# Kernel tuning notes

Measured on AMD Instinct MI355X. Metric: run time of the kernel, lower is better.

The kernel has to match this reference:

```python
import jax
import jax.numpy as jnp
from jax import lax
import numpy as np

# ---- static RPN config (mirrors init_kwargs) ----
STRIDES = (8, 16)
SIZES = ((32, 32), (16, 16))
SCALES = ((64.0 ** 2,), (128.0 ** 2,))
RATIOS = ((0.5, 1.0, 2.0), (0.5, 1.0, 2.0))
IMAGE_SIZE = (256, 256)
NMS_THRESH = 0.7
POST_NMS_TOP_N = 2000
NUM_LEVELS = 2
TOP_K_PER_LEVEL = POST_NMS_TOP_N // NUM_LEVELS  # padded NMS output slots per level


def _generate_anchors(stride, scales, ratios, size, image_size):
    """Anchors of shape (H*W*A, 4) in (x1,y1,x2,y2), clamped to image."""
    H, W = size
    cy = (np.arange(H, dtype=np.float32) + 0.5) * stride
    cx = (np.arange(W, dtype=np.float32) + 0.5) * stride
    ws, hs = [], []
    for s in scales:
        for r in ratios:
            ws.append(np.sqrt(s / r))
            hs.append(np.sqrt(s * r))
    ws = np.asarray(ws, np.float32)  # [A]
    hs = np.asarray(hs, np.float32)
    cxg, cyg = np.meshgrid(cx, cy)  # [H, W]
    x1 = cxg[..., None] - 0.5 * ws
    y1 = cyg[..., None] - 0.5 * hs
    x2 = cxg[..., None] + 0.5 * ws
    y2 = cyg[..., None] + 0.5 * hs
    a = np.stack([x1, y1, x2, y2], axis=-1)  # [H, W, A, 4]
    a[..., 0] = np.clip(a[..., 0], 0, image_size[0])
    a[..., 1] = np.clip(a[..., 1], 0, image_size[1])
    a[..., 2] = np.clip(a[..., 2], 0, image_size[0])
    a[..., 3] = np.clip(a[..., 3], 0, image_size[1])
    return a.reshape(-1, 4).astype(np.float32)


ANCHORS = [
    _generate_anchors(STRIDES[i], SCALES[i], RATIOS[i], SIZES[i], IMAGE_SIZE)
    for i in range(NUM_LEVELS)
]


def conv2d(x, w, b, padding):
    y = lax.conv_general_dilated(
        x, w, window_strides=(1, 1), padding=padding,
        dimension_numbers=("NCHW", "OIHW", "NCHW"))
    return y + b[None, :, None, None]


def decode_boxes(anchors, deltas):
    """Standard R-CNN box decode. anchors [N,4], deltas [..., N, 4]."""
    wa = anchors[:, 2] - anchors[:, 0]
    ha = anchors[:, 3] - anchors[:, 1]
    cxa = anchors[:, 0] + 0.5 * wa
    cya = anchors[:, 1] + 0.5 * ha
    dx, dy, dw, dh = deltas[..., 0], deltas[..., 1], deltas[..., 2], deltas[..., 3]
    cx = dx * wa + cxa
    cy = dy * ha + cya
    w = jnp.exp(dw) * wa
    h = jnp.exp(dh) * ha
    return jnp.stack([cx - 0.5 * w, cy - 0.5 * h, cx + 0.5 * w, cy + 0.5 * h], axis=-1)


def clamp_boxes(b):
    return jnp.stack([
        jnp.clip(b[..., 0], 0.0, IMAGE_SIZE[0]),
        jnp.clip(b[..., 1], 0.0, IMAGE_SIZE[1]),
        jnp.clip(b[..., 2], 0.0, IMAGE_SIZE[0]),
        jnp.clip(b[..., 3], 0.0, IMAGE_SIZE[1]),
    ], axis=-1)


def _pairwise_iou(b):
    # b: [N, 4] -> [N, N] IoU (torchvision convention, no +1)
    area = (b[:, 2] - b[:, 0]) * (b[:, 3] - b[:, 1])
    lt = jnp.maximum(b[:, None, :2], b[None, :, :2])
    rb = jnp.minimum(b[:, None, 2:], b[None, :, 2:])
    wh = jnp.clip(rb - lt, 0.0)
    inter = wh[..., 0] * wh[..., 1]
    return inter / (area[:, None] + area[None, :] - inter)


def nms_padded(boxes, scores, thresh, top_k):
    """Exact greedy NMS; returns (top_k,4) boxes and (top_k,) scores padded with -1."""
    N = boxes.shape[0]
    order = jnp.argsort(-scores)
    b = boxes[order]
    s = scores[order]
    iou = _pairwise_iou(b)  # [N, N]

    def body(supp, xs):
        row, i = xs
        keep_i = jnp.logical_not(supp[i])
        supp = supp | (keep_i & (row > thresh) & (jnp.arange(N) > i))
        return supp, keep_i

    _, keep = lax.scan(body, jnp.zeros((N,), bool), (iou, jnp.arange(N)))
    rank = jnp.cumsum(keep) - 1  # position among kept, in score order
    slot = jnp.where(keep & (rank < top_k), rank, top_k)  # overflow -> dump row
    out_b = jnp.full((top_k + 1, 4), -1.0, boxes.dtype).at[slot].set(b)
    out_s = jnp.full((top_k + 1,), -1.0, scores.dtype).at[slot].set(s)
    return out_b[:top_k], out_s[:top_k]


def _rpn_level(feat, anchors, conv_w, conv_b, cls_w, cls_b, reg_w, reg_b):
    x = jax.nn.relu(conv2d(feat, conv_w, conv_b, "SAME"))
    cls = conv2d(x, cls_w, cls_b, "VALID")              # [BS, A, H, W]
    reg = conv2d(x, reg_w, reg_b, "VALID")              # [BS, 4A, H, W]
    BS, A, H, W = cls.shape
    cls = cls.transpose(0, 2, 3, 1).reshape(BS, -1)                      # [BS, HWA]
    reg = reg.transpose(0, 2, 3, 1).reshape(BS, H, W, A, 4).reshape(BS, -1, 4)
    boxes = clamp_boxes(decode_boxes(anchors, lax.stop_gradient(reg)))   # [BS, HWA, 4]
    scores = jax.nn.sigmoid(lax.stop_gradient(cls))                      # [BS, HWA]
    kb, ks = jax.vmap(lambda bb, ss: nms_padded(bb, ss, NMS_THRESH, TOP_K_PER_LEVEL))(boxes, scores)
    return kb, ks


def setup_inputs() -> dict:
    key = jax.random.key(0)
    ks = jax.random.split(key, 5)
    C = 256
    A = 3
    return {
        "feat0": jax.random.normal(ks[0], (4, C, 32, 32), jnp.float32),
        "feat1": jax.random.normal(ks[1], (4, C, 16, 16), jnp.float32),
        "conv_w": 0.01 * jax.random.normal(ks[2], (C, C, 3, 3), jnp.float32),
        "conv_b": jnp.zeros((C,), jnp.float32),
        "cls_w": 0.01 * jax.random.normal(ks[3], (A, C, 1, 1), jnp.float32),
        "cls_b": jnp.zeros((A,), jnp.float32),
        "reg_w": 0.01 * jax.random.normal(ks[4], (4 * A, C, 1, 1), jnp.float32),
        "reg_b": jnp.zeros((4 * A,), jnp.float32),
    }


def reference(feat0, feat1, conv_w, conv_b, cls_w, cls_b, reg_w, reg_b):
    feats = [feat0, feat1]
    kb_all, ks_all = [], []
    for i in range(NUM_LEVELS):
        kb, ks = _rpn_level(feats[i], jnp.asarray(ANCHORS[i]),
                            conv_w, conv_b, cls_w, cls_b, reg_w, reg_b)
        kb_all.append(kb)
        ks_all.append(ks)
    bboxes = jnp.concatenate(kb_all, axis=1)   # [BS, POST_NMS_TOP_N, 4]
    scores = jnp.concatenate(ks_all, axis=1)   # [BS, POST_NMS_TOP_N]
    idx = jnp.argsort(-scores, axis=1)         # descending; -1 pads go last
    bboxes = jnp.take_along_axis(bboxes, idx[..., None], axis=1)
    return bboxes
```

## Files before the change

kernel.cpp:

```cpp
#include <hip/hip_runtime.h>
#include <math.h>


__global__ __launch_bounds__(256, 4) void conv3_sk_u(
    const float* __restrict__ feat0, const float* __restrict__ feat1,
    const float* __restrict__ conv_w,
    double* __restrict__ part0, double* __restrict__ part1)
{
  __shared__ float Ald[2][16][64];
  __shared__ float Bld[2][16][64];
  const int t = threadIdx.x;
  const int bid = blockIdx.x;
  const float* feat;
  double* part;
  int oc_t, p_t, k_base, hw_sh, w_sh, H;
  if (bid < 1024) {
    int kc = bid >> 8;
    feat = feat0; part = part0 + (size_t)kc * 4096 * 256;
    oc_t = bid & 3; p_t = (bid >> 2) & 63;
    k_base = kc * 576; hw_sh = 10; w_sh = 5; H = 32;
  } else {
    int b2 = bid - 1024;
    int kc = b2 >> 6;
    feat = feat1; part = part1 + (size_t)kc * 1024 * 256;
    oc_t = b2 & 3; p_t = (b2 >> 2) & 15;
    k_base = kc * 576; hw_sh = 8; w_sh = 4; H = 16;
  }
  const int oc_base = oc_t * 64;
  const int p_base  = p_t * 64;
  const int wmask = H - 1, hwmask = (1 << hw_sh) - 1;
  const int skk = t >> 4;
  const int q4  = (t & 15) * 4;

  float a_r[4], b_r[4];
  auto load_tile = [&](int kt) {
    const int k0 = k_base + kt * 16;
    const float* wrow = conv_w + (size_t)(oc_base + q4) * 2304 + (k0 + skk);
#pragma unroll
    for (int u = 0; u < 4; ++u) a_r[u] = wrow[(size_t)u * 2304];
    int p = p_base + q4;
    int b = p >> hw_sh, pin = p & hwmask;
    int y = pin >> w_sh, x0 = pin & wmask;
    int k = k0 + skk;
    int ic = k / 9, rr = k - ic * 9;
    int ky = rr / 3, kx = rr - ky * 3;
    int iy = y + ky - 1;
    const float* frow = feat + (((b << 8) + ic) << hw_sh) + (iy << w_sh);
    bool yok = (unsigned)iy < (unsigned)H;
#pragma unroll
    for (int u = 0; u < 4; ++u) {
      int ix = x0 + u + kx - 1;
      b_r[u] = (yok && (unsigned)ix < (unsigned)H) ? frow[ix] : 0.f;
    }
  };

  const int ty4 = (t >> 4) * 4;
  const int tx4 = (t & 15) * 4;
  double acc[4][4] = {};

  load_tile(0);
  for (int kt = 0; kt < 36; ++kt) {
    const int buf = kt & 1;
    *(float4*)&Ald[buf][skk][q4] = make_float4(a_r[0], a_r[1], a_r[2], a_r[3]);
    *(float4*)&Bld[buf][skk][q4] = make_float4(b_r[0], b_r[1], b_r[2], b_r[3]);
    __syncthreads();
    if (kt + 1 < 36) load_tile(kt + 1);
#pragma unroll
    for (int kk = 0; kk < 16; ++kk) {
      float4 av = *(const float4*)&Ald[buf][kk][ty4];
      float4 bv = *(const float4*)&Bld[buf][kk][tx4];
      double ad[4] = {(double)av.x, (double)av.y, (double)av.z, (double)av.w};
      double bd[4] = {(double)bv.x, (double)bv.y, (double)bv.z, (double)bv.w};
#pragma unroll
      for (int i = 0; i < 4; ++i)
#pragma unroll
        for (int j = 0; j < 4; ++j) acc[i][j] += ad[i] * bd[j];
    }
  }
#pragma unroll
  for (int j = 0; j < 4; ++j) {
    int p = p_base + tx4 + j;
    double* row = part + (size_t)p * 256 + oc_base + ty4;
    *(double2*)&row[0] = make_double2(acc[0][j], acc[1][j]);
    *(double2*)&row[2] = make_double2(acc[2][j], acc[3][j]);
  }
}

__global__ __launch_bounds__(256) void rhd_k(
    const double* __restrict__ part0, const double* __restrict__ part1,
    const float* __restrict__ conv_b,
    const float* __restrict__ cls_w, const float* __restrict__ cls_b,
    const float* __restrict__ reg_w, const float* __restrict__ reg_b,
    float* __restrict__ box0, float* __restrict__ sc0,
    float* __restrict__ box1, float* __restrict__ sc1)
{
  int wid = (blockIdx.x * 256 + threadIdx.x) >> 6;
  int lane = threadIdx.x & 63;
  int lvl = wid >= 4096;
  const double* part = lvl ? part1 : part0;
  int p = lvl ? wid - 4096 : wid;
  int M = lvl ? 1024 : 4096;
  double s4[4];
  {
    float4 bv = ((const float4*)conv_b)[lane];
    s4[0] = (double)bv.x; s4[1] = (double)bv.y;
    s4[2] = (double)bv.z; s4[3] = (double)bv.w;
  }
#pragma unroll
  for (int ks = 0; ks < 4; ++ks) {
    const double2* pr = (const double2*)(part + (size_t)ks * M * 256 + (size_t)p * 256);
    double2 a = pr[2 * lane], b = pr[2 * lane + 1];
    s4[0] += a.x; s4[1] += a.y; s4[2] += b.x; s4[3] += b.y;
  }
  float xv[4];
#pragma unroll
  for (int q = 0; q < 4; ++q) {
    float f = (float)s4[q];
    xv[q] = f > 0.f ? f : 0.f;
  }
  double acc[15];
#pragma unroll
  for (int o = 0; o < 15; ++o) {
    const float* wr = (o < 3) ? (cls_w + o * 256) : (reg_w + (o - 3) * 256);
    float4 wv = ((const float4*)wr)[lane];
    acc[o] = (double)wv.x * (double)xv[0] + (double)wv.y * (double)xv[1] +
             (double)wv.z * (double)xv[2] + (double)wv.w * (double)xv[3];
  }
#pragma unroll
  for (int d = 1; d < 64; d <<= 1)
#pragma unroll
    for (int o = 0; o < 15; ++o)
      acc[o] += __shfl_xor(acc[o], d, 64);
  if (lane < 3) {
    int a = lane;
    float cls = (float)(acc[a] + (double)cls_b[a]);
    float score = 1.f / (1.f + expf(-cls));
    float dx = (float)(acc[3 + a * 4 + 0] + (double)reg_b[a * 4 + 0]);
    float dy = (float)(acc[3 + a * 4 + 1] + (double)reg_b[a * 4 + 1]);
    float dw = (float)(acc[3 + a * 4 + 2] + (double)reg_b[a * 4 + 2]);
    float dh = (float)(acc[3 + a * 4 + 3] + (double)reg_b[a * 4 + 3]);
    int hw_sh = lvl ? 8 : 10, w_sh = lvl ? 4 : 5, Wd = lvl ? 16 : 32;
    float S = lvl ? 16.f : 8.f;
    double scale = lvl ? 16384.0 : 4096.0;
    int b = p >> hw_sh, pin = p & ((1 << hw_sh) - 1);
    int y = pin >> w_sh, x = pin & (Wd - 1);
    double ratio = (a == 0) ? 0.5 : (a == 1 ? 1.0 : 2.0);
    float w_a = (float)sqrt(scale / ratio);
    float h_a = (float)sqrt(scale * ratio);
    float cx = ((float)x + 0.5f) * S;
    float cy = ((float)y + 0.5f) * S;
    float x1 = cx - 0.5f * w_a, y1 = cy - 0.5f * h_a;
    float x2 = cx + 0.5f * w_a, y2 = cy + 0.5f * h_a;
    x1 = fminf(fmaxf(x1, 0.f), 256.f); y1 = fminf(fmaxf(y1, 0.f), 256.f);
    x2 = fminf(fmaxf(x2, 0.f), 256.f); y2 = fminf(fmaxf(y2, 0.f), 256.f);
    float wa = x2 - x1, ha = y2 - y1;
    float cxa = x1 + 0.5f * wa, cya = y1 + 0.5f * ha;
    float ncx = dx * wa + cxa;
    float ncy = dy * ha + cya;
    float nw = expf(dw) * wa;
    float nh = expf(dh) * ha;
    float bx1 = ncx - 0.5f * nw, by1 = ncy - 0.5f * nh;
    float bx2 = ncx + 0.5f * nw, by2 = ncy + 0.5f * nh;
    bx1 = fminf(fmaxf(bx1, 0.f), 256.f); by1 = fminf(fmaxf(by1, 0.f), 256.f);
    bx2 = fminf(fmaxf(bx2, 0.f), 256.f); by2 = fminf(fmaxf(by2, 0.f), 256.f);
    int n = pin * 3 + a;
    if (lvl) {
      ((float4*)box1)[(size_t)b * 768 + n] = make_float4(bx1, by1, bx2, by2);
      sc1[b * 768 + n] = score;
    } else {
      ((float4*)box0)[(size_t)b * 3072 + n] = make_float4(bx1, by1, bx2, by2);
      sc0[b * 3072 + n] = score;
    }
  }
}

__global__ __launch_bounds__(256) void sort_level_k(
    const float* __restrict__ sc0, const float* __restrict__ box0,
    float* __restrict__ ssc0, float* __restrict__ sbox0,
    const float* __restrict__ sc1, const float* __restrict__ box1,
    float* __restrict__ ssc1, float* __restrict__ sbox1)
{
  __shared__ __align__(16) float s[3072];
  int z = blockIdx.x;
  const float *sc, *box; float *ssc, *sbox; int N, b, c;
  if (z < 48) { sc = sc0; box = box0; ssc = ssc0; sbox = sbox0; N = 3072; b = z / 12; c = z % 12; }
  else { int z2 = z - 48; sc = sc1; box = box1; ssc = ssc1; sbox = sbox1; N = 768; b = z2 / 3; c = z2 % 3; }
  const float* scb = sc + (size_t)b * N;
  for (int j = threadIdx.x; j < N; j += 256) s[j] = scb[j];
  __syncthreads();
  int i = c * 256 + threadIdx.x;
  float si = s[i];
  int rank = 0;
  const float4* sv = (const float4*)s;
  for (int j4 = 0; j4 < (N >> 2); ++j4) {
    float4 v = sv[j4];
    int j = j4 * 4;
    rank += (v.x > si) || (v.x == si && (j + 0) < i);
    rank += (v.y > si) || (v.y == si && (j + 1) < i);
    rank += (v.z > si) || (v.z == si && (j + 2) < i);
    rank += (v.w > si) || (v.w == si && (j + 3) < i);
  }
  ssc[(size_t)b * N + rank] = si;
  float4 bi = ((const float4*)box)[(size_t)b * N + i];
  ((float4*)sbox)[(size_t)b * N + rank] = bi;
}

__global__ __launch_bounds__(256) void mask_col_k(
    const float* __restrict__ sbox0, const float* __restrict__ sbox1,
    unsigned long long* __restrict__ mask0, unsigned long long* __restrict__ mask1,
    unsigned long long* __restrict__ colD0, unsigned long long* __restrict__ colD1)
{
  int bid = blockIdx.x;
  if (bid < 2448) {
    __shared__ float4 bj[64];
    const float* sbox; unsigned long long* mask; int N, words, w, i_ch, b;
    if (bid < 2304) {
      sbox = sbox0; mask = mask0; N = 3072; words = 48;
      w = bid % 48; int r = bid / 48; i_ch = r % 12; b = r / 12;
    } else {
      int z = bid - 2304;
      sbox = sbox1; mask = mask1; N = 768; words = 12;
      w = z % 12; int r = z / 12; i_ch = r % 3; b = r / 3;
    }
    int i = i_ch * 256 + threadIdx.x;
    if (threadIdx.x < 64)
      bj[threadIdx.x] = ((const float4*)sbox)[(size_t)b * N + w * 64 + threadIdx.x];
    __syncthreads();
    float4 bi = ((const float4*)sbox)[(size_t)b * N + i];
    float ai = (bi.z - bi.x) * (bi.w - bi.y);
    unsigned long long m = 0ull;
#pragma unroll 16
    for (int jj = 0; jj < 64; ++jj) {
      int j = w * 64 + jj;
      float4 bv = bj[jj];
      float lx = fmaxf(bi.x, bv.x), ly = fmaxf(bi.y, bv.y);
      float rx = fminf(bi.z, bv.z), ry = fminf(bi.w, bv.w);
      float iw = fmaxf(rx - lx, 0.f), ih = fmaxf(ry - ly, 0.f);
      float inter = iw * ih;
      float aj = (bv.z - bv.x) * (bv.w - bv.y);
      float iou = inter / (ai + aj - inter);
      if ((iou > 0.7f) & (j > i)) m |= (1ull << jj);
    }
    mask[((size_t)b * N + i) * words + w] = m;
  } else {
    __shared__ float4 tb[4][64];
    int sub = threadIdx.x >> 6, lane = threadIdx.x & 63;
    const float* sbox; unsigned long long* colD; int N, tile, b;
    if (bid < 2496) {
      int unit = (bid - 2448) * 4 + sub;
      sbox = sbox0; colD = colD0; N = 3072;
      tile = unit % 48; b = unit / 48;
    } else {
      int unit = (bid - 2496) * 4 + sub;
      sbox = sbox1; colD = colD1; N = 768;
      tile = unit % 12; b = unit / 12;
    }
    tb[sub][lane] = ((const float4*)sbox)[(size_t)b * N + tile * 64 + lane];
    __syncthreads();
    float4 bq = tb[sub][lane];
    float aq = (bq.z - bq.x) * (bq.w - bq.y);
    unsigned long long col = 0ull;
#pragma unroll 16
    for (int ii = 0; ii < 64; ++ii) {
      float4 bi = tb[sub][ii];
      float lx = fmaxf(bq.x, bi.x), ly = fmaxf(bq.y, bi.y);
      float rx = fminf(bq.z, bi.z), ry = fminf(bq.w, bi.w);
      float iw = fmaxf(rx - lx, 0.f), ih = fmaxf(ry - ly, 0.f);
      float inter = iw * ih;
      float ai = (bi.z - bi.x) * (bi.w - bi.y);
      float iou = inter / (aq + ai - inter);
      if ((iou > 0.7f) & (lane > ii)) col |= (1ull << ii);
    }
    colD[(size_t)b * N + tile * 64 + lane] = col;
  }
}

__global__ __launch_bounds__(64) void nms_scan_k(
    const float* __restrict__ ssc0, const float* __restrict__ sbox0,
    const unsigned long long* __restrict__ mask0,
    const unsigned long long* __restrict__ colD0,
    const float* __restrict__ ssc1, const float* __restrict__ sbox1,
    const unsigned long long* __restrict__ mask1,
    const unsigned long long* __restrict__ colD1,
    float* __restrict__ cb, float* __restrict__ cs)
{
  int z = blockIdx.x;
  int lvl = z >> 2, b = z & 3;
  int N = lvl ? 768 : 3072;
  int words = lvl ? 12 : 48;
  const float* ssc = (lvl ? ssc1 : ssc0) + (size_t)b * N;
  const float4* sbox = ((const float4*)(lvl ? sbox1 : sbox0)) + (size_t)b * N;
  const unsigned long long* mask = (lvl ? mask1 : mask0) + (size_t)b * N * words;
  const unsigned long long* colD = (lvl ? colD1 : colD0) + (size_t)b * N;
  const int lane = threadIdx.x;
  float* csb = cs + (size_t)b * 2000 + lvl * 1000;
  float4* cbb = (float4*)(cb + ((size_t)b * 2000 + lvl * 1000) * 4);
  for (int q = lane; q < 1000; q += 64) {
    csb[q] = -1.f;
    cbb[q] = make_float4(-1.f, -1.f, -1.f, -1.f);
  }
  unsigned long long removed = 0ull;
  int kept_base = 0;
  unsigned long long colv = colD[lane];
  float sc_i = ssc[lane];
  float4 bx_i = sbox[lane];
  for (int t = 0; t < words; ++t) {
    unsigned long long wr = __shfl(removed, t);
    bool doprop = (lane > t) && (lane < words);
    const unsigned long long* row = mask + (size_t)t * 64 * words + lane;
    unsigned long long v[32];
    if (doprop) {
#pragma unroll
      for (int s = 0; s < 32; ++s) v[s] = row[(size_t)s * words];
    }
    bool sup = (wr >> lane) & 1ull;
    unsigned long long col = colv;
#pragma unroll
    for (int i = 0; i < 64; ++i) {
      unsigned long long supv = __ballot(sup);
      bool keep_i = !((supv >> i) & 1ull);
      sup = sup | (keep_i & ((col >> i) & 1ull));
    }
    unsigned long long keep64 = ~__ballot(sup);
    if (!sup) {
      int rank = kept_base + __popcll(keep64 & ((1ull << lane) - 1ull));
      if (rank < 1000) { csb[rank] = sc_i; cbb[rank] = bx_i; }
    }
    kept_base += __popcll(keep64);
    if (kept_base >= 1000) break;
    if (t + 1 >= words) break;
    {
      int i2 = (t + 1) * 64 + lane;
      colv = colD[i2]; sc_i = ssc[i2]; bx_i = sbox[i2];
    }
    if (doprop) {
      unsigned long long acc = removed;
#pragma unroll
      for (int s = 0; s < 32; ++s)
        acc |= (((keep64 >> s) & 1ull) ? v[s] : 0ull);
#pragma unroll
      for (int s = 0; s < 32; ++s) v[s] = row[(size_t)(32 + s) * words];
#pragma unroll
      for (int s = 0; s < 32; ++s)
        acc |= (((keep64 >> (32 + s)) & 1ull) ? v[s] : 0ull);
      removed = acc;
    }
  }
}

__global__ __launch_bounds__(256) void final_sort_k(
    const float* __restrict__ cs, const float* __restrict__ cb,
    float* __restrict__ out)
{
  __shared__ __align__(16) float s[2000];
  int b = blockIdx.x >> 3, c = blockIdx.x & 7;
  const float* csb = cs + (size_t)b * 2000;
  for (int j = threadIdx.x; j < 2000; j += 256) s[j] = csb[j];
  __syncthreads();
  if (threadIdx.x >= 250) return;
  int li = c * 250 + threadIdx.x;
  float si = s[li];
  int rank = 0;
  const float4* sv = (const float4*)s;
  for (int j4 = 0; j4 < 500; ++j4) {
    float4 v = sv[j4];
    int j = j4 * 4;
    rank += (v.x > si) || (v.x == si && (j + 0) < li);
    rank += (v.y > si) || (v.y == si && (j + 1) < li);
    rank += (v.z > si) || (v.z == si && (j + 2) < li);
    rank += (v.w > si) || (v.w == si && (j + 3) < li);
  }
  float4 bi = ((const float4*)cb)[(size_t)b * 2000 + li];
  ((float4*)out)[(size_t)b * 2000 + rank] = bi;
}

extern "C" void kernel_launch(void* const* d_in, const int* in_sizes, int n_in,
                              void* d_out, int out_size, void* d_ws, size_t ws_size,
                              hipStream_t stream) {
  const float* feat0  = (const float*)d_in[0];
  const float* feat1  = (const float*)d_in[1];
  const float* conv_w = (const float*)d_in[2];
  const float* conv_b = (const float*)d_in[3];
  const float* cls_w  = (const float*)d_in[4];
  const float* cls_b  = (const float*)d_in[5];
  const float* reg_w  = (const float*)d_in[6];
  const float* reg_b  = (const float*)d_in[7];

  char* p = (char*)d_ws;
  auto alloc = [&](size_t bytes) {
    char* r = p;
    p += (bytes + 255) & ~(size_t)255;
    return r;
  };
  double* part0 = (double*)alloc((size_t)4 * 4096 * 256 * 8);
  double* part1 = (double*)alloc((size_t)4 * 1024 * 256 * 8);
  float* box0 = (float*)alloc((size_t)4 * 3072 * 16);
  float* sc0  = (float*)alloc((size_t)4 * 3072 * 4);
  float* box1 = (float*)alloc((size_t)4 * 768 * 16);
  float* sc1  = (float*)alloc((size_t)4 * 768 * 4);
  float* sbox0 = (float*)alloc((size_t)4 * 3072 * 16);
  float* ssc0  = (float*)alloc((size_t)4 * 3072 * 4);
  float* sbox1 = (float*)alloc((size_t)4 * 768 * 16);
  float* ssc1  = (float*)alloc((size_t)4 * 768 * 4);
  unsigned long long* mask0 = (unsigned long long*)alloc((size_t)4 * 3072 * 48 * 8);
  unsigned long long* mask1 = (unsigned long long*)alloc((size_t)4 * 768 * 12 * 8);
  unsigned long long* colD0 = (unsigned long long*)alloc((size_t)4 * 3072 * 8);
  unsigned long long* colD1 = (unsigned long long*)alloc((size_t)4 * 768 * 8);
  float* cb = (float*)alloc((size_t)4 * 2000 * 16);
  float* cs = (float*)alloc((size_t)4 * 2000 * 4);

  conv3_sk_u<<<1280, 256, 0, stream>>>(feat0, feat1, conv_w, part0, part1);
  rhd_k<<<1280, 256, 0, stream>>>(part0, part1, conv_b, cls_w, cls_b,
                                  reg_w, reg_b, box0, sc0, box1, sc1);
  sort_level_k<<<60, 256, 0, stream>>>(sc0, box0, ssc0, sbox0,
                                       sc1, box1, ssc1, sbox1);
  mask_col_k<<<2508, 256, 0, stream>>>(sbox0, sbox1, mask0, mask1, colD0, colD1);
  nms_scan_k<<<8, 64, 0, stream>>>(ssc0, sbox0, mask0, colD0,
                                   ssc1, sbox1, mask1, colD1, cb, cs);
  final_sort_k<<<32, 256, 0, stream>>>(cs, cb, (float*)d_out);
}
```

Baseline: 547.1 us.

## Replace serial 64-step NMS ballot chain with iterative fixed-point resolution

Within each 64-box NMS tile, the strictly sequential 64-iteration ballot loop is replaced by a fixed-point iteration. Each round keeps every box whose higher-scored suppressors (colv) have all been removed, then removes boxes suppressed by the newly kept ones, so the number of rounds follows the dependency chain depth instead of always being 64. The full 64-row mask block is now prefetched into two register arrays before the resolve, rather than loading the second half afterwards, to hide load latency. That doubles live 64-bit registers per lane, and a data-dependent loop adds branch overhead.

Result: faster. 533.2 us (-2.5%).

```diff
diff --git a/kernel.cpp b/kernel.cpp
--- a/kernel.cpp
+++ b/kernel.cpp
@@ -308,21 +308,29 @@
     unsigned long long wr = __shfl(removed, t);
     bool doprop = (lane > t) && (lane < words);
     const unsigned long long* row = mask + (size_t)t * 64 * words + lane;
-    unsigned long long v[32];
+    unsigned long long v1[32], v2[32];
     if (doprop) {
 #pragma unroll
-      for (int s = 0; s < 32; ++s) v[s] = row[(size_t)s * words];
-    }
-    bool sup = (wr >> lane) & 1ull;
-    unsigned long long col = colv;
-#pragma unroll
-    for (int i = 0; i < 64; ++i) {
-      unsigned long long supv = __ballot(sup);
-      bool keep_i = !((supv >> i) & 1ull);
-      sup = sup | (keep_i & ((col >> i) & 1ull));
-    }
-    unsigned long long keep64 = ~__ballot(sup);
-    if (!sup) {
+      for (int s = 0; s < 32; ++s) v1[s] = row[(size_t)s * words];
+#pragma unroll
+      for (int s = 0; s < 32; ++s) v2[s] = row[(size_t)(32 + s) * words];
+    }
+    bool rm = (wr >> lane) & 1ull;
+    bool kp = false;
+    unsigned long long Rv = wr;
+    unsigned long long Kv = 0ull;
+    while (true) {
+      bool F = (!rm) && (!kp) && ((colv & ~Rv) == 0ull);
+      unsigned long long Fv = __ballot(F);
+      if (Fv == 0ull) break;
+      kp = kp || F;
+      Kv |= Fv;
+      bool newr = (!rm) && (!kp) && ((colv & Fv) != 0ull);
+      rm = rm || newr;
+      Rv = __ballot(rm);
+    }
+    unsigned long long keep64 = Kv;
+    if (kp) {
       int rank = kept_base + __popcll(keep64 & ((1ull << lane) - 1ull));
       if (rank < 1000) { csb[rank] = sc_i; cbb[rank] = bx_i; }
     }
@@ -337,12 +345,10 @@
       unsigned long long acc = removed;
 #pragma unroll
       for (int s = 0; s < 32; ++s)
-        acc |= (((keep64 >> s) & 1ull) ? v[s] : 0ull);
-#pragma unroll
-      for (int s = 0; s < 32; ++s) v[s] = row[(size_t)(32 + s) * words];
+        acc |= (((keep64 >> s) & 1ull) ? v1[s] : 0ull);
 #pragma unroll
       for (int s = 0; s < 32; ++s)
-        acc |= (((keep64 >> (32 + s)) & 1ull) ? v[s] : 0ull);
+        acc |= (((keep64 >> (32 + s)) & 1ull) ? v2[s] : 0ull);
       removed = acc;
     }
   }
```
